# Kernel tuning notes

Measured on AMD Instinct MI355X. Metric: run time of the kernel, lower is better.

## Reference

```python
import jax, jax.numpy as jnp
import numpy as np

D_MODEL = 1024
N_HEAD = 16
SEQ_LEN = 4096


def setup_inputs() -> dict:
    key = jax.random.key(0)
    ks = jax.random.split(key, 5)
    s = 0.02
    return {
        "x": jax.random.normal(ks[0], (SEQ_LEN, D_MODEL), dtype=jnp.float32),
        "w_qkv": jax.random.normal(ks[1], (D_MODEL, 3 * D_MODEL), dtype=jnp.float32) * s,
        "b_qkv": jnp.zeros((3 * D_MODEL,), dtype=jnp.float32),
        "w_o": jax.random.normal(ks[2], (D_MODEL, D_MODEL), dtype=jnp.float32) * s,
        "b_o": jnp.zeros((D_MODEL,), dtype=jnp.float32),
    }


def reference(x, w_qkv, b_qkv, w_o, b_o):
    seq_len, d_model = x.shape
    n_head = N_HEAD
    d_h = d_model // n_head

    qkv = x @ w_qkv + b_qkv                                  # [S, 3D]
    q, k, v = jnp.split(qkv, 3, axis=-1)                     # each [S, D]
    # [S, D] -> [H, S, d_h]
    q = q.reshape(seq_len, n_head, d_h).transpose(1, 0, 2)
    k = k.reshape(seq_len, n_head, d_h).transpose(1, 0, 2)
    v = v.reshape(seq_len, n_head, d_h).transpose(1, 0, 2)

    sim = jnp.einsum("hsd,htd->hst", q, k) / jnp.sqrt(jnp.float32(d_h))  # [H, S, S]
    causal = jnp.tril(jnp.ones((seq_len, seq_len), dtype=bool))[None]    # [1, S, S]
    neg_inf = jnp.finfo(sim.dtype).min
    sim = jnp.where(causal, sim, neg_inf)
    attn = jax.nn.softmax(sim, axis=-1)                                  # [H, S, S]
    out = jnp.einsum("hst,htd->hsd", attn, v)                            # [H, S, d_h]
    out = out.transpose(1, 0, 2).reshape(seq_len, d_model)               # [S, D]
    return out @ w_o + b_o
```

## Files before the change

### kernel.cpp

```cpp
#include <hip/hip_runtime.h>
#include <hip/hip_bf16.h>
#include <stdint.h>

typedef __bf16 bf16_t;
typedef __bf16 bf16x8 __attribute__((ext_vector_type(8)));
typedef float f32x4 __attribute__((ext_vector_type(4)));
typedef float f32x16 __attribute__((ext_vector_type(16)));

#define SEQ_LEN 4096
#define D_MODEL 1024
#define N_HEAD 16



__device__ __forceinline__ void gload_lds16(const void* g, void* lds) {
  __builtin_amdgcn_global_load_lds(
      (__attribute__((address_space(1))) void*)(g),
      (__attribute__((address_space(3))) void*)(lds), 16, 0, 0);
}

__device__ __forceinline__ unsigned short f2bfu(float f) {
  __bf16 h = (__bf16)f;
  return __builtin_bit_cast(unsigned short, h);
}

__device__ __forceinline__ unsigned cvt_pk_bf16(float a, float b) {
  unsigned r;
  asm("v_cvt_pk_bf16_f32 %0, %1, %2" : "=v"(r) : "v"(a), "v"(b));
  return r;
}

#define CBAR() asm volatile("" ::: "memory")


__global__ __launch_bounds__(256) void prep_fused(const float* __restrict__ x,
                                                  bf16_t* __restrict__ xh,
                                                  const float* __restrict__ w_qkv,
                                                  bf16_t* __restrict__ wqkvT,
                                                  const float* __restrict__ w_o,
                                                  bf16_t* __restrict__ woT) {
  __shared__ float tile[64][65];
  const int b = blockIdx.x;
  if (b < 4096) {
    int i = (b * 256 + threadIdx.x) * 4;
    float4 v = *(const float4*)(x + i);
    unsigned int lo = (unsigned)f2bfu(v.x) | ((unsigned)f2bfu(v.y) << 16);
    unsigned int hi = (unsigned)f2bfu(v.z) | ((unsigned)f2bfu(v.w) << 16);
    uint2 pk; pk.x = lo; pk.y = hi;
    *(uint2*)(xh + i) = pk;
    return;
  }
  const float* W;
  bf16_t* Wt;
  int C, bi;
  if (b < 4864) { W = w_qkv; Wt = wqkvT; C = 3072; bi = b - 4096; }
  else          { W = w_o;   Wt = woT;   C = 1024; bi = b - 4864; }
  const int R = 1024;
  const int tc = C >> 6;
  const int bc = bi % tc;
  const int br = bi / tc;
  #pragma unroll
  for (int p = 0; p < 16; ++p) {
    int idx = p * 256 + threadIdx.x;
    int i = idx >> 6, j = idx & 63;
    tile[i][j] = W[(size_t)(br * 64 + i) * C + bc * 64 + j];
  }
  __syncthreads();
  #pragma unroll
  for (int p = 0; p < 16; ++p) {
    int idx = p * 256 + threadIdx.x;
    int jj = idx >> 6, ii = idx & 63;
    Wt[(size_t)(bc * 64 + jj) * R + br * 64 + ii] = (bf16_t)tile[ii][jj];
  }
}


__device__ __forceinline__ void stage_half(const bf16_t* src, char* ldsbase,
                                           int w, int srow, int schunk) {
  const bf16_t* s0 = src + (size_t)(w * 8 + srow) * 1024 + schunk * 8;
  char* d0 = ldsbase + w * 1024;
  gload_lds16(s0, d0);
  gload_lds16(s0 + 64 * 1024, d0 + 8192);
}

__global__ __launch_bounds__(512, 2) void gemm1_8p(const bf16_t* __restrict__ A,
                                                   const bf16_t* __restrict__ Bt,
                                                   const float* __restrict__ bias,
                                                   bf16_t* __restrict__ qfout,
                                                   bf16_t* __restrict__ kfout,
                                                   bf16_t* __restrict__ vfout) {
  __shared__ char ldsbuf[131072];
  const int tid = threadIdx.x;
  const int lane = tid & 63;
  const int w = tid >> 6;
  const int wm = w >> 2;
  const int wn = w & 3;
  const int i16 = lane & 15;
  const int g = lane >> 4;
  const int hi = lane >> 5;
  const int bswz = (blockIdx.x & 7) * 24 + (blockIdx.x >> 3);
  const int bm = bswz / 12;
  const int bn = bswz % 12;

  const int srow = lane >> 3;
  const int schunk = (lane & 7) ^ (hi << 1);
  const int s5 = ((i16 >> 2) & 1) << 5;

  auto stA = [&](int buf, int half, int kt) {
    stage_half(A + (size_t)(bm * 256 + half * 128) * 1024 + kt * 64,
               ldsbuf + buf * 32768 + half * 16384, w, srow, schunk);
  };
  auto stB = [&](int buf, int half, int kt) {
    stage_half(Bt + (size_t)(bn * 256 + half * 128) * 1024 + kt * 64,
               ldsbuf + 65536 + buf * 32768 + half * 16384, w, srow, schunk);
  };

  f32x4 acc[8][4];
  #pragma unroll
  for (int m = 0; m < 8; ++m)
    #pragma unroll
    for (int n = 0; n < 4; ++n)
      acc[m][n] = (f32x4){0.f, 0.f, 0.f, 0.f};

  const int browbase = (wn & 1) * 64;

  stA(0, 0, 0); stA(0, 1, 0); stB(0, 0, 0); stB(0, 1, 0);
  stB(1, 0, 1); stB(1, 1, 1);
  asm volatile("s_waitcnt vmcnt(4)" ::: "memory");
  CBAR(); __builtin_amdgcn_s_barrier(); CBAR();

  bf16x8 bfr[4][2];

  for (int i = 0; i < 8; ++i) {
    const int t1 = 2 * i + 1, t2 = 2 * i + 2, t3 = 2 * i + 3;
    #pragma unroll
    for (int p = 0; p < 8; ++p) {
      const int buf = p >> 2;
      const int q = p & 3;
      const char* aB = ldsbuf + buf * 32768 + wm * 16384;
      const char* bB = ldsbuf + 65536 + buf * 32768 + (wn >> 1) * 16384;
      if (q == 0) {
        #pragma unroll
        for (int n = 0; n < 4; ++n)
          #pragma unroll
          for (int ks = 0; ks < 2; ++ks) {
            int U = (browbase + n * 16 + i16) * 128 + ks * 64 + g * 16;
            bfr[n][ks] = *(const bf16x8*)(bB + (U ^ s5));
          }
      }
      bf16x8 af[2][2];
      #pragma unroll
      for (int mm = 0; mm < 2; ++mm)
        #pragma unroll
        for (int ks = 0; ks < 2; ++ks) {
          int U = ((q * 2 + mm) * 16 + i16) * 128 + ks * 64 + g * 16;
          af[mm][ks] = *(const bf16x8*)(aB + (U ^ s5));
        }
      if (p == 0)      stA(1, 0, t1);
      else if (p == 1) stA(1, 1, t1);
      else if (p == 2) { if (t2 < 16) stB(0, 0, t2); }
      else if (p == 3) { if (t2 < 16) stB(0, 1, t2); }
      else if (p == 4) { if (t2 < 16) stA(0, 0, t2); }
      else if (p == 5) { if (t2 < 16) stA(0, 1, t2); }
      else if (p == 6) { if (t3 < 16) stB(1, 0, t3); }
      else             { if (t3 < 16) stB(1, 1, t3); }

      CBAR(); __builtin_amdgcn_s_barrier(); CBAR();

      __builtin_amdgcn_s_setprio(1);
      #pragma unroll
      for (int mm = 0; mm < 2; ++mm)
        #pragma unroll
        for (int n = 0; n < 4; ++n)
          #pragma unroll
          for (int ks = 0; ks < 2; ++ks)
            acc[q * 2 + mm][n] = __builtin_amdgcn_mfma_f32_16x16x32_bf16(
                af[mm][ks], bfr[n][ks], acc[q * 2 + mm][n], 0, 0, 0);
      __builtin_amdgcn_s_setprio(0);

      if (p == 3) {
        if (i == 7) asm volatile("s_waitcnt vmcnt(0)" ::: "memory");
        else        asm volatile("s_waitcnt vmcnt(4)" ::: "memory");
      } else if (p == 7 && i < 7) {
        asm volatile("s_waitcnt vmcnt(4)" ::: "memory");
      }
      CBAR(); __builtin_amdgcn_s_barrier(); CBAR();
    }
  }

  #pragma unroll
  for (int m = 0; m < 8; ++m) {
    #pragma unroll
    for (int n = 0; n < 4; ++n) {
      int col = bn * 256 + wn * 64 + n * 16 + i16;
      float bv = bias[col];
      int row0 = bm * 256 + wm * 128 + m * 16 + g * 4;
      if (col < 2048) {
        const bool isK = (col >= 1024);
        const float scl = isK ? 0.18033688011112042f : 1.0f;
        bf16_t* base = isK ? kfout : qfout;
        int dg = col & 1023;
        int hh = dg >> 6, d = dg & 63;
        int ks = d >> 4, hib = (d >> 3) & 1, e = d & 7;
        int t = row0 >> 5, l0 = row0 & 31;
        bf16_t* fp = base + (size_t)hh * 262144 + t * 2048 + ks * 512 +
                     hib * 256 + l0 * 8 + e;
        #pragma unroll
        for (int r = 0; r < 4; ++r)
          fp[r * 8] = (bf16_t)((acc[m][n][r] + bv) * scl);
      } else {
        int dg = col - 2048;
        int hh = dg >> 6, dh = dg & 63;
        int dt = dh >> 5, l31v = dh & 31;
        int t = row0 >> 5, inner = row0 & 31;
        int g2 = inner >> 4, hiv = (inner >> 3) & 1, e0 = inner & 7;
        uint2 pk;
        pk.x = cvt_pk_bf16(acc[m][n][0] + bv, acc[m][n][1] + bv);
        pk.y = cvt_pk_bf16(acc[m][n][2] + bv, acc[m][n][3] + bv);
        *(uint2*)(vfout + (size_t)hh * 262144 + t * 2048 + dt * 1024 +
                  g2 * 512 + hiv * 256 + l31v * 8 + e0) = pk;
      }
    }
  }
}


__global__ __launch_bounds__(256) void gemm_bt(const bf16_t* __restrict__ A,
                                               const bf16_t* __restrict__ Bt,
                                               const float* __restrict__ bias,
                                               float* __restrict__ Cout,
                                               int M, int N, int K) {
  __shared__ bf16_t As[128 * 32];
  __shared__ bf16_t Bs[128 * 32];
  const int tid = threadIdx.x;
  const int lane = tid & 63;
  const int w = tid >> 6;
  const int wr = (w >> 1) * 64;
  const int wc = (w & 1) * 64;
  const int i16 = lane & 15;
  const int g = lane >> 4;
  const int ntn = N >> 7;
  const int nwg = gridDim.x;
  const int bswz = (blockIdx.x & 7) * (nwg >> 3) + (blockIdx.x >> 3);
  const int bm = bswz / ntn;
  const int bn = bswz % ntn;
  const bf16_t* Abase = A + (size_t)(bm * 128) * K;
  const bf16_t* Bbase = Bt + (size_t)(bn * 128) * K;

  f32x4 acc[4][4];
  #pragma unroll
  for (int m = 0; m < 4; ++m)
    #pragma unroll
    for (int n = 0; n < 4; ++n)
      acc[m][n] = (f32x4){0.f, 0.f, 0.f, 0.f};

  for (int kt = 0; kt < K; kt += 32) {
    __syncthreads();
    #pragma unroll
    for (int p = 0; p < 2; ++p) {
      int idx = p * 256 + tid;
      int row = idx >> 2, ch = idx & 3;
      gload_lds16(Abase + (size_t)row * K + kt + ch * 8, (char*)As + idx * 16);
      gload_lds16(Bbase + (size_t)row * K + kt + ch * 8, (char*)Bs + idx * 16);
    }
    __syncthreads();
    bf16x8 af[4], bq[4];
    #pragma unroll
    for (int m = 0; m < 4; ++m)
      af[m] = *(const bf16x8*)(As + (wr + m * 16 + i16) * 32 + g * 8);
    #pragma unroll
    for (int n = 0; n < 4; ++n)
      bq[n] = *(const bf16x8*)(Bs + (wc + n * 16 + i16) * 32 + g * 8);
    #pragma unroll
    for (int m = 0; m < 4; ++m)
      #pragma unroll
      for (int n = 0; n < 4; ++n)
        acc[m][n] = __builtin_amdgcn_mfma_f32_16x16x32_bf16(af[m], bq[n], acc[m][n], 0, 0, 0);
  }

  #pragma unroll
  for (int m = 0; m < 4; ++m) {
    #pragma unroll
    for (int n = 0; n < 4; ++n) {
      int col = bn * 128 + wc + n * 16 + i16;
      float bv = bias ? bias[col] : 0.f;
      int row0 = bm * 128 + wr + m * 16 + g * 4;
      #pragma unroll
      for (int r = 0; r < 4; ++r)
        Cout[(size_t)(row0 + r) * N + col] = acc[m][n][r] + bv;
    }
  }
}


__global__ __launch_bounds__(256) void attn_fwd(const bf16_t* __restrict__ qf_,
                                                const bf16_t* __restrict__ kf,
                                                const bf16_t* __restrict__ vf,
                                                bf16_t* __restrict__ aout) {
  __shared__ float Obuf[2][32][68];
  __shared__ float lpart[4][2][32];
  const int tid = threadIdx.x;
  const int w = tid >> 6;
  const int lane = tid & 63;
  const int l31 = lane & 31;
  const int hi = lane >> 5;
  const int bid = blockIdx.x;
  const int h = ((bid & 7) << 1) | ((bid >> 3) & 1);
  const int j = 127 - (bid >> 4);
  const int qg0 = j * 32;

  const bf16_t* qp = qf_ + (size_t)h * 262144 + (size_t)j * 2048 + hi * 256 + l31 * 8;
  bf16x8 qf[4];
  #pragma unroll
  for (int ks = 0; ks < 4; ++ks)
    qf[ks] = *(const bf16x8*)(qp + ks * 512);

  const bf16_t* kp = kf + (size_t)h * 262144 + hi * 256 + l31 * 8;
  const bf16_t* vp = vf + (size_t)h * 262144 + hi * 256 + l31 * 8;

  f32x16 ot0, ot1;
  #pragma unroll
  for (int r = 0; r < 16; ++r) { ot0[r] = 0.f; ot1[r] = 0.f; }
  float l_run = 0.f;

  const int nt = j + 1;
  bf16x8 kc[4], kn[4], vc[4];
  #pragma unroll
  for (int ks = 0; ks < 4; ++ks) {
    kc[ks] = *(const bf16x8*)(kp + w * 2048 + ks * 512);
    kn[ks] = kc[ks];
  }

  for (int t = w; t < nt; t += 4) {
    #pragma unroll
    for (int i = 0; i < 4; ++i) {
      int dt = i >> 1, g2 = i & 1;
      vc[i] = *(const bf16x8*)(vp + (size_t)t * 2048 + dt * 1024 + g2 * 512);
    }
    if (t + 4 < nt) {
      #pragma unroll
      for (int ks = 0; ks < 4; ++ks)
        kn[ks] = *(const bf16x8*)(kp + (size_t)(t + 4) * 2048 + ks * 512);
    }

    f32x16 s;
    #pragma unroll
    for (int r = 0; r < 16; ++r) s[r] = 0.f;
    __builtin_amdgcn_s_setprio(1);
    #pragma unroll
    for (int ks = 0; ks < 4; ++ks)
      s = __builtin_amdgcn_mfma_f32_32x32x16_bf16(kc[ks], qf[ks], s, 0, 0, 0);
    __builtin_amdgcn_s_setprio(0);

    if (t == nt - 1) {
      #pragma unroll
      for (int r = 0; r < 16; ++r) {
        int c = (r & 3) + 8 * (r >> 2) + 4 * hi;
        if (c > l31) s[r] = -1e30f;
      }
    }

    #pragma unroll
    for (int r = 0; r < 16; ++r)
      s[r] = __builtin_amdgcn_exp2f(s[r]);

    float sm[8];
    #pragma unroll
    for (int r = 0; r < 8; ++r) sm[r] = s[r] + s[r + 8];
    #pragma unroll
    for (int r = 0; r < 4; ++r) sm[r] = sm[r] + sm[r + 4];
    l_run += (sm[0] + sm[1]) + (sm[2] + sm[3]);

    bf16x8 pb[2];
    #pragma unroll
    for (int g2 = 0; g2 < 2; ++g2) {
      const int r0 = g2 * 8;
      unsigned a0 = cvt_pk_bf16(s[r0 + 0], s[r0 + 1]);
      unsigned a1 = cvt_pk_bf16(s[r0 + 2], s[r0 + 3]);
      unsigned b0 = cvt_pk_bf16(s[r0 + 4], s[r0 + 5]);
      unsigned b1 = cvt_pk_bf16(s[r0 + 6], s[r0 + 7]);
      unsigned X0 = hi ? a0 : b0;
      unsigned X1 = hi ? a1 : b1;
      unsigned Y0 = __shfl_xor(X0, 32);
      unsigned Y1 = __shfl_xor(X1, 32);
      uint4 f;
      f.x = hi ? Y0 : a0;
      f.y = hi ? Y1 : a1;
      f.z = hi ? b0 : Y0;
      f.w = hi ? b1 : Y1;
      pb[g2] = __builtin_bit_cast(bf16x8, f);
    }

    __builtin_amdgcn_s_setprio(1);
    ot0 = __builtin_amdgcn_mfma_f32_32x32x16_bf16(vc[0], pb[0], ot0, 0, 0, 0);
    ot0 = __builtin_amdgcn_mfma_f32_32x32x16_bf16(vc[1], pb[1], ot0, 0, 0, 0);
    ot1 = __builtin_amdgcn_mfma_f32_32x32x16_bf16(vc[2], pb[0], ot1, 0, 0, 0);
    ot1 = __builtin_amdgcn_mfma_f32_32x32x16_bf16(vc[3], pb[1], ot1, 0, 0, 0);
    __builtin_amdgcn_s_setprio(0);

    #pragma unroll
    for (int ks = 0; ks < 4; ++ks) kc[ks] = kn[ks];
  }

  lpart[w][hi][l31] = l_run;
  if (w >= 2) {
    #pragma unroll
    for (int dt = 0; dt < 2; ++dt) {
      const f32x16& o = dt ? ot1 : ot0;
      #pragma unroll
      for (int rq = 0; rq < 4; ++rq) {
        f32x4 qd;
        qd[0] = o[4 * rq + 0];
        qd[1] = o[4 * rq + 1];
        qd[2] = o[4 * rq + 2];
        qd[3] = o[4 * rq + 3];
        *(f32x4*)&Obuf[w - 2][l31][dt * 32 + 8 * rq + 4 * hi] = qd;
      }
    }
  }
  __syncthreads();
  if (w < 2) {
    #pragma unroll
    for (int dt = 0; dt < 2; ++dt) {
      const f32x16& o = dt ? ot1 : ot0;
      #pragma unroll
      for (int rq = 0; rq < 4; ++rq) {
        f32x4 qd = *(const f32x4*)&Obuf[w][l31][dt * 32 + 8 * rq + 4 * hi];
        qd[0] += o[4 * rq + 0];
        qd[1] += o[4 * rq + 1];
        qd[2] += o[4 * rq + 2];
        qd[3] += o[4 * rq + 3];
        *(f32x4*)&Obuf[w][l31][dt * 32 + 8 * rq + 4 * hi] = qd;
      }
    }
  }
  __syncthreads();
  #pragma unroll
  for (int iter = 0; iter < 8; ++iter) {
    int qq = w * 8 + iter;
    float sum = Obuf[0][qq][lane] + Obuf[1][qq][lane];
    float lst = lpart[0][0][qq] + lpart[0][1][qq] + lpart[1][0][qq] + lpart[1][1][qq] +
                lpart[2][0][qq] + lpart[2][1][qq] + lpart[3][0][qq] + lpart[3][1][qq];
    aout[(size_t)(qg0 + qq) * 1024 + h * 64 + lane] = (bf16_t)(sum / lst);
  }
}


extern "C" void kernel_launch(void* const* d_in, const int* in_sizes, int n_in,
                              void* d_out, int out_size, void* d_ws, size_t ws_size,
                              hipStream_t stream) {
  const float* x     = (const float*)d_in[0];
  const float* w_qkv = (const float*)d_in[1];
  const float* b_qkv = (const float*)d_in[2];
  const float* w_o   = (const float*)d_in[3];
  const float* b_o   = (const float*)d_in[4];

  char* ws = (char*)d_ws;
  bf16_t* xh    = (bf16_t*)(ws);
  bf16_t* wqkvT = (bf16_t*)(ws + 8388608);
  bf16_t* woT   = (bf16_t*)(ws + 14680064);
  bf16_t* qfb   = (bf16_t*)(ws + 16777216);
  bf16_t* kfb   = (bf16_t*)(ws + 25165824);
  bf16_t* vfb   = (bf16_t*)(ws + 33554432);
  bf16_t* aout  = (bf16_t*)(ws + 41943040);

  prep_fused<<<5120, 256, 0, stream>>>(x, xh, w_qkv, wqkvT, w_o, woT);

  gemm1_8p<<<192, 512, 0, stream>>>(xh, wqkvT, b_qkv, qfb, kfb, vfb);

  attn_fwd<<<N_HEAD * (SEQ_LEN / 32), 256, 0, stream>>>(qfb, kfb, vfb, aout);

  gemm_bt<<<(4096 / 128) * (1024 / 128), 256, 0, stream>>>(
      aout, woT, b_o, (float*)d_out, 4096, 1024, 1024);
}
```

Measured before the change: 132.6 us.

## Software-pipeline QK^T one tile ahead of softmax and PV in attention loop

Restructures the causal attention inner loop so the QK^T MFMAs for tile t+4 are issued before the exp, row-sum and bf16 packing of tile t. K tiles are now prefetched two iterations ahead, and the loop is unrolled by two with ping-ponged score and register buffers. The K register buffer is reused to hold the V tile after its scores are computed, which keeps register pressure down. The aim is to overlap matrix-core work with the VALU and transcendental softmax work. In exchange, the V load now lands closer to its use, and the extra live accumulator may increase register pressure.

```diff
diff --git a/kernel.cpp b/kernel.cpp
--- a/kernel.cpp
+++ b/kernel.cpp
@@ -324,82 +324,110 @@
   float l_run = 0.f;
 
   const int nt = j + 1;
-  bf16x8 kc[4], kn[4], vc[4];
-  #pragma unroll
-  for (int ks = 0; ks < 4; ++ks) {
-    kc[ks] = *(const bf16x8*)(kp + w * 2048 + ks * 512);
-    kn[ks] = kc[ks];
-  }
-
-  for (int t = w; t < nt; t += 4) {
-    #pragma unroll
-    for (int i = 0; i < 4; ++i) {
-      int dt = i >> 1, g2 = i & 1;
-      vc[i] = *(const bf16x8*)(vp + (size_t)t * 2048 + dt * 1024 + g2 * 512);
-    }
-    if (t + 4 < nt) {
-      #pragma unroll
-      for (int ks = 0; ks < 4; ++ks)
-        kn[ks] = *(const bf16x8*)(kp + (size_t)(t + 4) * 2048 + ks * 512);
-    }
-
-    f32x16 s;
-    #pragma unroll
-    for (int r = 0; r < 16; ++r) s[r] = 0.f;
-    __builtin_amdgcn_s_setprio(1);
+
+  bf16x8 kA[4], kB[4];
+  f32x16 sA, sB;
+
+  #pragma unroll
+  for (int ks = 0; ks < 4; ++ks)
+    kA[ks] = *(const bf16x8*)(kp + (size_t)w * 2048 + ks * 512);
+  {
+    f32x16 z;
+    #pragma unroll
+    for (int r = 0; r < 16; ++r) z[r] = 0.f;
     #pragma unroll
     for (int ks = 0; ks < 4; ++ks)
-      s = __builtin_amdgcn_mfma_f32_32x32x16_bf16(kc[ks], qf[ks], s, 0, 0, 0);
-    __builtin_amdgcn_s_setprio(0);
-
-    if (t == nt - 1) {
-      #pragma unroll
-      for (int r = 0; r < 16; ++r) {
-        int c = (r & 3) + 8 * (r >> 2) + 4 * hi;
-        if (c > l31) s[r] = -1e30f;
-      }
-    }
-
-    #pragma unroll
-    for (int r = 0; r < 16; ++r)
-      s[r] = __builtin_amdgcn_exp2f(s[r]);
-
-    float sm[8];
-    #pragma unroll
-    for (int r = 0; r < 8; ++r) sm[r] = s[r] + s[r + 8];
-    #pragma unroll
-    for (int r = 0; r < 4; ++r) sm[r] = sm[r] + sm[r + 4];
-    l_run += (sm[0] + sm[1]) + (sm[2] + sm[3]);
-
-    bf16x8 pb[2];
-    #pragma unroll
-    for (int g2 = 0; g2 < 2; ++g2) {
-      const int r0 = g2 * 8;
-      unsigned a0 = cvt_pk_bf16(s[r0 + 0], s[r0 + 1]);
-      unsigned a1 = cvt_pk_bf16(s[r0 + 2], s[r0 + 3]);
-      unsigned b0 = cvt_pk_bf16(s[r0 + 4], s[r0 + 5]);
-      unsigned b1 = cvt_pk_bf16(s[r0 + 6], s[r0 + 7]);
-      unsigned X0 = hi ? a0 : b0;
-      unsigned X1 = hi ? a1 : b1;
-      unsigned Y0 = __shfl_xor(X0, 32);
-      unsigned Y1 = __shfl_xor(X1, 32);
-      uint4 f;
-      f.x = hi ? Y0 : a0;
-      f.y = hi ? Y1 : a1;
-      f.z = hi ? b0 : Y0;
-      f.w = hi ? b1 : Y1;
-      pb[g2] = __builtin_bit_cast(bf16x8, f);
-    }
-
-    __builtin_amdgcn_s_setprio(1);
-    ot0 = __builtin_amdgcn_mfma_f32_32x32x16_bf16(vc[0], pb[0], ot0, 0, 0, 0);
-    ot0 = __builtin_amdgcn_mfma_f32_32x32x16_bf16(vc[1], pb[1], ot0, 0, 0, 0);
-    ot1 = __builtin_amdgcn_mfma_f32_32x32x16_bf16(vc[2], pb[0], ot1, 0, 0, 0);
-    ot1 = __builtin_amdgcn_mfma_f32_32x32x16_bf16(vc[3], pb[1], ot1, 0, 0, 0);
-    __builtin_amdgcn_s_setprio(0);
-
-    #pragma unroll
-    for (int ks = 0; ks < 4; ++ks) kc[ks] = kn[ks];
+      z = __builtin_amdgcn_mfma_f32_32x32x16_bf16(kA[ks], qf[ks], z, 0, 0, 0);
+    sA = z;
+  }
+  if (w + 4 < nt) {
+    #pragma unroll
+    for (int ks = 0; ks < 4; ++ks)
+      kB[ks] = *(const bf16x8*)(kp + (size_t)(w + 4) * 2048 + ks * 512);
+  } else {
+    #pragma unroll
+    for (int ks = 0; ks < 4; ++ks)
+      kB[ks] = kA[ks];
+  }
+  sB = sA;
+
+  int t = w;
+  auto step = [&](f32x16& SCUR, f32x16& SNXT, bf16x8 (&KN)[4], bf16x8 (&KF)[4]) {
+    if (t < nt) {
+      if (t + 8 < nt) {
+        #pragma unroll
+        for (int ks = 0; ks < 4; ++ks)
+          KF[ks] = *(const bf16x8*)(kp + (size_t)(t + 8) * 2048 + ks * 512);
+      }
+      if (t + 4 < nt) {
+        f32x16 z;
+        #pragma unroll
+        for (int r = 0; r < 16; ++r) z[r] = 0.f;
+        __builtin_amdgcn_s_setprio(1);
+        #pragma unroll
+        for (int ks = 0; ks < 4; ++ks)
+          z = __builtin_amdgcn_mfma_f32_32x32x16_bf16(KN[ks], qf[ks], z, 0, 0, 0);
+        __builtin_amdgcn_s_setprio(0);
+        SNXT = z;
+      }
+      #pragma unroll
+      for (int i = 0; i < 4; ++i) {
+        int dt = i >> 1, g2 = i & 1;
+        KN[i] = *(const bf16x8*)(vp + (size_t)t * 2048 + dt * 1024 + g2 * 512);
+      }
+
+      if (t == nt - 1) {
+        #pragma unroll
+        for (int r = 0; r < 16; ++r) {
+          int c = (r & 3) + 8 * (r >> 2) + 4 * hi;
+          if (c > l31) SCUR[r] = -1e30f;
+        }
+      }
+
+      #pragma unroll
+      for (int r = 0; r < 16; ++r)
+        SCUR[r] = __builtin_amdgcn_exp2f(SCUR[r]);
+
+      float sm[8];
+      #pragma unroll
+      for (int r = 0; r < 8; ++r) sm[r] = SCUR[r] + SCUR[r + 8];
+      #pragma unroll
+      for (int r = 0; r < 4; ++r) sm[r] = sm[r] + sm[r + 4];
+      l_run += (sm[0] + sm[1]) + (sm[2] + sm[3]);
+
+      bf16x8 pb[2];
+      #pragma unroll
+      for (int g2 = 0; g2 < 2; ++g2) {
+        const int r0 = g2 * 8;
+        unsigned a0 = cvt_pk_bf16(SCUR[r0 + 0], SCUR[r0 + 1]);
+        unsigned a1 = cvt_pk_bf16(SCUR[r0 + 2], SCUR[r0 + 3]);
+        unsigned b0 = cvt_pk_bf16(SCUR[r0 + 4], SCUR[r0 + 5]);
+        unsigned b1 = cvt_pk_bf16(SCUR[r0 + 6], SCUR[r0 + 7]);
+        unsigned X0 = hi ? a0 : b0;
+        unsigned X1 = hi ? a1 : b1;
+        unsigned Y0 = __shfl_xor(X0, 32);
+        unsigned Y1 = __shfl_xor(X1, 32);
+        uint4 f;
+        f.x = hi ? Y0 : a0;
+        f.y = hi ? Y1 : a1;
+        f.z = hi ? b0 : Y0;
+        f.w = hi ? b1 : Y1;
+        pb[g2] = __builtin_bit_cast(bf16x8, f);
+      }
+
+      __builtin_amdgcn_s_setprio(1);
+      ot0 = __builtin_amdgcn_mfma_f32_32x32x16_bf16(KN[0], pb[0], ot0, 0, 0, 0);
+      ot0 = __builtin_amdgcn_mfma_f32_32x32x16_bf16(KN[1], pb[1], ot0, 0, 0, 0);
+      ot1 = __builtin_amdgcn_mfma_f32_32x32x16_bf16(KN[2], pb[0], ot1, 0, 0, 0);
+      ot1 = __builtin_amdgcn_mfma_f32_32x32x16_bf16(KN[3], pb[1], ot1, 0, 0, 0);
+      __builtin_amdgcn_s_setprio(0);
+    }
+    t += 4;
+  };
+
+  while (t < nt) {
+    step(sA, sB, kB, kA);
+    step(sB, sA, kA, kB);
   }
 
   lpart[w][hi][l31] = l_run;
```

After: 139.1 us. 4.8% more time.
